# Optimization experiments

Measured on AMD Instinct MI355X. Metric: run time of the kernel, lower is better.

## Reference

```python
import jax, jax.numpy as jnp
import numpy as np

N_NODES = 50000
N_EDGES = 800000
IN_FEATS = 128
H_FEATS = 128
NUM_CLASSES = 64


def _linear_params(key, fan_in, fan_out):
    kw, kb = jax.random.split(key)
    bound = 1.0 / np.sqrt(fan_in)
    W = jax.random.uniform(kw, (fan_out, fan_in), minval=-bound, maxval=bound, dtype=jnp.float32)
    b = jax.random.uniform(kb, (fan_out,), minval=-bound, maxval=bound, dtype=jnp.float32)
    return W, b


def setup_inputs() -> dict:
    key = jax.random.key(0)
    k_feat, k_src, k_dst, k1, k2, k3 = jax.random.split(key, 6)
    in_feat = jax.random.normal(k_feat, (N_NODES, IN_FEATS), dtype=jnp.float32)
    src = jax.random.randint(k_src, (N_EDGES,), 0, N_NODES, dtype=jnp.int32)
    dst = jax.random.randint(k_dst, (N_EDGES,), 0, N_NODES, dtype=jnp.int32)
    W1, b1 = _linear_params(k1, IN_FEATS, H_FEATS)
    W2, b2 = _linear_params(k2, H_FEATS, H_FEATS)
    W3, b3 = _linear_params(k3, H_FEATS, NUM_CLASSES)
    return {"in_feat": in_feat, "W1": W1, "b1": b1, "W2": W2, "b2": b2,
            "W3": W3, "b3": b3, "src": src, "dst": dst}


def reference(in_feat, W1, b1, W2, b2, W3, b3, src, dst):
    N = in_feat.shape[0]

    def gin_layer(x, W, b):
        # DGL GINConv with eps=0: (x + sum of in-neighbor messages) -> Linear
        agg = jax.ops.segment_sum(x[src], dst, num_segments=N)  # [N, d]
        return jax.nn.relu((x + agg) @ W.T + b)

    h = gin_layer(in_feat, W1, b1)
    h = gin_layer(h, W2, b2)
    h = gin_layer(h, W3, b3)
    return h
```

## Files before the change

kernel.cpp:

```cpp
#include <hip/hip_runtime.h>

typedef _Float16 half8 __attribute__((ext_vector_type(8)));
typedef float floatx4 __attribute__((ext_vector_type(4)));
typedef unsigned int uintx4 __attribute__((ext_vector_type(4)));

union AB { uint4 u; half8 h; };
union H2 { unsigned int u; _Float16 h[2]; };
union US16 { uintx4 u[2]; unsigned short s[16]; };

#define CAPLOG 6
#define CAP 64

__global__ __launch_bounds__(256) void histA_k(const int* __restrict__ dst,
                                               int* __restrict__ histG, int E, int nbins) {
    __shared__ int h[256];
    int t = threadIdx.x;
    h[t] = 0;
    __syncthreads();
    int per = (E + 255) / 256;
    int beg = blockIdx.x * per;
    int end = min(E, beg + per);
    for (int e = beg + t; e < end; e += 256)
        atomicAdd(&h[dst[e] >> 8], 1);
    __syncthreads();
    for (int i = t; i < nbins; i += 256)
        histG[i * 256 + blockIdx.x] = h[i];
}

__global__ __launch_bounds__(1024) void scan1_k(const int* __restrict__ x,
                                                int* __restrict__ inc,
                                                int* __restrict__ partial, int n) {
    __shared__ int sd[1024];
    int t = threadIdx.x;
    int v = blockIdx.x * 1024 + t;
    sd[t] = (v < n) ? x[v] : 0;
    __syncthreads();
    for (int off = 1; off < 1024; off <<= 1) {
        int val = (t >= off) ? sd[t - off] : 0;
        __syncthreads();
        sd[t] += val;
        __syncthreads();
    }
    if (v < n) inc[v] = sd[t];
    if (t == 1023) partial[blockIdx.x] = sd[1023];
}

__global__ void scan2_k(int* __restrict__ partial, int nb) {
    int lane = threadIdx.x;
    int v = (lane < nb) ? partial[lane] : 0;
    for (int off = 1; off < 64; off <<= 1) {
        int n = __shfl_up(v, off, 64);
        if (lane >= off) v += n;
    }
    int ex = __shfl_up(v, 1, 64);
    if (lane == 0) ex = 0;
    if (lane < nb) partial[lane] = ex;
}

__global__ void scan3_excl_k(const int* __restrict__ inc, const int* __restrict__ partial,
                             const int* __restrict__ orig, int* __restrict__ excl, int n) {
    int v = blockIdx.x * blockDim.x + threadIdx.x;
    if (v < n) excl[v] = inc[v] + partial[v >> 10] - orig[v];
}

__global__ __launch_bounds__(256) void scatterA_k(const int* __restrict__ src,
                                                  const int* __restrict__ dst,
                                                  const int* __restrict__ excl,
                                                  unsigned int* __restrict__ binned,
                                                  int E, int nbins) {
    __shared__ int cur[256];
    int t = threadIdx.x;
    for (int i = t; i < nbins; i += 256) cur[i] = excl[i * 256 + blockIdx.x];
    __syncthreads();
    int per = (E + 255) / 256;
    int beg = blockIdx.x * per;
    int end = min(E, beg + per);
    for (int e = beg + t; e < end; e += 256) {
        int d = dst[e];
        int s = src[e];
        int pos = atomicAdd(&cur[d >> 8], 1);
        binned[pos] = ((unsigned int)(d & 255) << 16) | (unsigned int)s;
    }
}

__global__ __launch_bounds__(256) void binB_k(const unsigned int* __restrict__ binned,
                                              const int* __restrict__ excl,
                                              unsigned short* __restrict__ col,
                                              int* __restrict__ cnt,
                                              int N, int E, int nbins) {
    __shared__ unsigned short lcol[256 * CAP];
    __shared__ int lcnt[256];
    int t = threadIdx.x;
    int b = blockIdx.x;
    unsigned int* lcol32 = (unsigned int*)lcol;
    for (int i = t; i < 256 * CAP / 2; i += 256) lcol32[i] = 0xFFFFFFFFu;
    lcnt[t] = 0;
    __syncthreads();
    int beg = excl[b * 256];
    int end = (b == nbins - 1) ? E : excl[(b + 1) * 256];
    for (int e = beg + t; e < end; e += 256) {
        unsigned int u = binned[e];
        int dl = u >> 16;
        int pos = atomicAdd(&lcnt[dl], 1);
        if (pos < CAP) lcol[(dl << CAPLOG) + pos] = (unsigned short)(u & 0xFFFFu);
    }
    __syncthreads();
    int base = b << 8;
    int nodes = min(256, N - base);
    uint4* colg = (uint4*)(col + ((size_t)base << CAPLOG));
    const uint4* coll = (const uint4*)lcol;
    for (int i = t; i < nodes * 8; i += 256) colg[i] = coll[i];
    for (int i = t; i < nodes; i += 256) cnt[base + i] = lcnt[i];
}

__global__ void init_k(const float* __restrict__ F, const float* __restrict__ W1,
                       const float* __restrict__ W2, const float* __restrict__ W3,
                       _Float16* __restrict__ hX, _Float16* __restrict__ W1h,
                       _Float16* __restrict__ W2h, _Float16* __restrict__ W3h,
                       _Float16* __restrict__ hB,
                       int n4f, int n4w1, int n4w2, int n4w3, int zoff4) {
    int i = blockIdx.x * blockDim.x + threadIdx.x;
    const float* X;
    _Float16* O;
    int j;
    if (i < n4f) { X = F; O = hX; j = i; }
    else if (i < n4f + n4w1) { X = W1; O = W1h; j = i - n4f; }
    else if (i < n4f + n4w1 + n4w2) { X = W2; O = W2h; j = i - n4f - n4w1; }
    else if (i < n4f + n4w1 + n4w2 + n4w3) { X = W3; O = W3h; j = i - n4f - n4w1 - n4w2; }
    else {
        int z = i - (n4f + n4w1 + n4w2 + n4w3);
        if (z < 16) ((uint4*)hX)[zoff4 + z] = make_uint4(0, 0, 0, 0);
        else if (z < 32) ((uint4*)hB)[zoff4 + z - 16] = make_uint4(0, 0, 0, 0);
        return;
    }
    float4 v = reinterpret_cast<const float4*>(X)[j];
    union { uint2 u; _Float16 h[4]; } o;
    o.h[0] = (_Float16)v.x; o.h[1] = (_Float16)v.y;
    o.h[2] = (_Float16)v.z; o.h[3] = (_Float16)v.w;
    reinterpret_cast<uint2*>(O)[j] = o.u;
}

__global__ __launch_bounds__(256) void aggregate_k(const _Float16* __restrict__ X,
                                                   const int* __restrict__ cnt,
                                                   const unsigned short* __restrict__ col,
                                                   _Float16* __restrict__ Y,
                                                   int nnodes) {
    int b = blockIdx.x;
    int q = (b & 7) >> 1;
    int ng = ((b >> 3) << 1) | (b & 1);
    int lane = threadIdx.x & 63;
    int fl = lane & 15;
    int node = ng * 16 + (threadIdx.x >> 6) * 4 + (lane >> 4);
    if (node >= nnodes) return;
    const unsigned int* X32 = (const unsigned int*)X;
    int qoff = q << 4;

    int deg = cnt[node];
    if (deg > CAP) deg = CAP;
    int degp = (deg + 15) & ~15;
    const unsigned short* c = col + ((size_t)node << CAPLOG);

    float a[8], bb[8];
#pragma unroll
    for (int j = 0; j < 8; j++) { a[j] = 0.f; bb[j] = 0.f; }

    for (int e = 0; e < degp; e += 16) {
        US16 ix;
        ix.u[0] = *reinterpret_cast<const uintx4*>(c + e);
        ix.u[1] = *reinterpret_cast<const uintx4*>(c + e + 8);
        H2 u[16];
#pragma unroll
        for (int j = 0; j < 16; j++) {
            int s = (int)ix.s[j];
            s = (s < nnodes) ? s : nnodes;
            u[j].u = X32[(size_t)s * 64 + qoff + fl];
        }
#pragma unroll
        for (int j = 0; j < 8; j++) {
            a[j] += (float)u[j].h[0] + (float)u[j + 8].h[0];
            bb[j] += (float)u[j].h[1] + (float)u[j + 8].h[1];
        }
    }

    H2 xs, r;
    xs.u = X32[(size_t)node * 64 + qoff + fl];
    float s0 = ((a[0] + a[1]) + (a[2] + a[3])) + ((a[4] + a[5]) + (a[6] + a[7]));
    float s1 = ((bb[0] + bb[1]) + (bb[2] + bb[3])) + ((bb[4] + bb[5]) + (bb[6] + bb[7]));
    r.h[0] = (_Float16)((float)xs.h[0] + s0);
    r.h[1] = (_Float16)((float)xs.h[1] + s1);
    __builtin_nontemporal_store(r.u, reinterpret_cast<unsigned int*>(Y) + (size_t)node * 64 + qoff + fl);
}

template <int NOUT, bool OUT_F32>
__global__ __launch_bounds__(256) void gemm_mfma_k(const _Float16* __restrict__ Y,
                                                   const _Float16* __restrict__ Wh,
                                                   const float* __restrict__ bias,
                                                   void* __restrict__ out, int nnodes) {
    constexpr int NT = NOUT / 16;
    constexpr int WSTR = 136;
    __shared__ _Float16 Wl[NOUT * WSTR];
    __shared__ float Bl[NOUT];

    const int t = threadIdx.x;
    for (int p = t; p < NOUT * 16; p += 256) {
        int f = p >> 4;
        int kq = (p & 15) * 8;
        uint4 u = *reinterpret_cast<const uint4*>(Wh + f * 128 + kq);
        *reinterpret_cast<uint4*>(&Wl[f * WSTR + kq]) = u;
    }
    if (t < NOUT) Bl[t] = bias[t];
    __syncthreads();

    const int wave = t >> 6;
    const int lane = t & 63;
    const int quad = lane >> 4;
    const int fcol = lane & 15;
    const int m_base = (blockIdx.x * 4 + wave) * 16;
    const int row = m_base + fcol;
    const bool rowok = row < nnodes;

    floatx4 acc[NT];
#pragma unroll
    for (int ft = 0; ft < NT; ft++) acc[ft] = (floatx4){0.f, 0.f, 0.f, 0.f};

    const uint4* Yrow = reinterpret_cast<const uint4*>(Y + (size_t)row * 128);
#pragma unroll
    for (int step = 0; step < 4; step++) {
        AB a;
        if (rowok) a.u = Yrow[step * 4 + quad];
        else       a.u = make_uint4(0u, 0u, 0u, 0u);
#pragma unroll
        for (int ft = 0; ft < NT; ft++) {
            half8 b = *reinterpret_cast<const half8*>(
                &Wl[(ft * 16 + fcol) * WSTR + step * 32 + quad * 8]);
            acc[ft] = __builtin_amdgcn_mfma_f32_16x16x32_f16(a.h, b, acc[ft], 0, 0, 0);
        }
    }

#pragma unroll
    for (int ft = 0; ft < NT; ft++) {
        int f = ft * 16 + fcol;
        float bv = Bl[f];
#pragma unroll
        for (int r = 0; r < 4; r++) {
            int node = m_base + quad * 4 + r;
            if (node < nnodes) {
                float v = fmaxf(acc[ft][r] + bv, 0.f);
                if (OUT_F32)
                    reinterpret_cast<float*>(out)[(size_t)node * NOUT + f] = v;
                else
                    reinterpret_cast<_Float16*>(out)[(size_t)node * NOUT + f] = (_Float16)v;
            }
        }
    }
}

extern "C" void kernel_launch(void* const* d_in, const int* in_sizes, int n_in,
                              void* d_out, int out_size, void* d_ws, size_t ws_size,
                              hipStream_t stream) {
    const float* in_feat = (const float*)d_in[0];
    const float* W1 = (const float*)d_in[1];
    const float* b1 = (const float*)d_in[2];
    const float* W2 = (const float*)d_in[3];
    const float* b2 = (const float*)d_in[4];
    const float* W3 = (const float*)d_in[5];
    const float* b3 = (const float*)d_in[6];
    const int* src = (const int*)d_in[7];
    const int* dst = (const int*)d_in[8];
    float* out = (float*)d_out;

    const int N = in_sizes[0] / 128;
    const int E = in_sizes[7];
    const int szW1 = in_sizes[1];
    const int szW2 = in_sizes[3];
    const int szW3 = in_sizes[5];
    const int nbins = (N + 255) >> 8;
    const int nhist = nbins * 256;

    char* p = (char*)d_ws;
    int* cnt = (int*)p;               p += (size_t)N * 4;
    unsigned short* col = (unsigned short*)p; p += (size_t)N * CAP * 2;
    int* histG = (int*)p;             p += (size_t)nhist * 4;
    int* incS = (int*)p;              p += (size_t)nhist * 4;
    int* excl = (int*)p;              p += (size_t)nhist * 4;
    int* partial = (int*)p;           p += 256;
    unsigned int* binned = (unsigned int*)p; p += (size_t)E * 4;
    _Float16* hX = (_Float16*)p;      p += (size_t)(N + 1) * 128 * 2;
    _Float16* hB = (_Float16*)p;      p += (size_t)(N + 1) * 128 * 2;
    _Float16* W1h = (_Float16*)p;     p += (size_t)szW1 * 2;
    _Float16* W2h = (_Float16*)p;     p += (size_t)szW2 * 2;
    _Float16* W3h = (_Float16*)p;     p += (size_t)szW3 * 2;

    const int nblk_scan = (nhist + 1023) / 1024;

    histA_k<<<256, 256, 0, stream>>>(dst, histG, E, nbins);
    scan1_k<<<nblk_scan, 1024, 0, stream>>>(histG, incS, partial, nhist);
    scan2_k<<<1, 64, 0, stream>>>(partial, nblk_scan);
    scan3_excl_k<<<(nhist + 255) / 256, 256, 0, stream>>>(incS, partial, histG, excl, nhist);
    scatterA_k<<<256, 256, 0, stream>>>(src, dst, excl, binned, E, nbins);
    binB_k<<<nbins, 256, 0, stream>>>(binned, excl, col, cnt, N, E, nbins);

    {
        int n4f = N * 128 / 4;
        int total = n4f + szW1 / 4 + szW2 / 4 + szW3 / 4 + 32;
        init_k<<<(total + 255) / 256, 256, 0, stream>>>(in_feat, W1, W2, W3,
                                                        hX, W1h, W2h, W3h, hB,
                                                        n4f, szW1 / 4, szW2 / 4, szW3 / 4,
                                                        N * 16);
    }

    const int ngrp = (N + 15) / 16;
    const int nblk_agg = 8 * ((ngrp + 1) / 2);
    const int nblk_gemm = (N + 63) / 64;
    aggregate_k<<<nblk_agg, 256, 0, stream>>>(hX, cnt, col, hB, N);
    gemm_mfma_k<128, false><<<nblk_gemm, 256, 0, stream>>>(hB, W1h, b1, hX, N);
    aggregate_k<<<nblk_agg, 256, 0, stream>>>(hX, cnt, col, hB, N);
    gemm_mfma_k<128, false><<<nblk_gemm, 256, 0, stream>>>(hB, W2h, b2, hX, N);
    aggregate_k<<<nblk_agg, 256, 0, stream>>>(hX, cnt, col, hB, N);
    gemm_mfma_k<64, true><<<nblk_gemm, 256, 0, stream>>>(hB, W3h, b3, out, N);
}
```

Measured before the change: 263.9 us.

## Reorder last GIN layer to GEMM-then-aggregate and fuse preprocessing kernels

For the final layer the code now applies the linear map first, (x+agg)W = xW + agg(xW), so the last aggregation gathers 64-wide fp16 rows instead of 128-wide. Bias and ReLU move into a new final aggregation kernel that writes fp32 output. The histogram and fp16 conversion kernels are merged into one launch, and the scan2/scan3 steps are folded into the scatter and binning kernels, removing several small launches. The aggregate kernel's mapping changes from quarter-row to half-row chunks per thread group with a different XCD-aware block swizzle. The reordering changes fp16 rounding order, since the GEMM output is rounded before summation.

```diff
diff --git a/kernel.cpp b/kernel.cpp
--- a/kernel.cpp
+++ b/kernel.cpp
@@ -11,115 +11,30 @@
 #define CAPLOG 6
 #define CAP 64
 
-__global__ __launch_bounds__(256) void histA_k(const int* __restrict__ dst,
-                                               int* __restrict__ histG, int E, int nbins) {
-    __shared__ int h[256];
+__global__ __launch_bounds__(256) void histA_init_k(
+    const int* __restrict__ dst, int* __restrict__ histG, int E, int nbins,
+    const float* __restrict__ F, const float* __restrict__ W1,
+    const float* __restrict__ W2, const float* __restrict__ W3,
+    _Float16* __restrict__ hX, _Float16* __restrict__ W1h,
+    _Float16* __restrict__ W2h, _Float16* __restrict__ W3h,
+    _Float16* __restrict__ hZ,
+    int n4f, int n4w1, int n4w2, int n4w3, int zoffX4, int zoffZ4) {
     int t = threadIdx.x;
-    h[t] = 0;
-    __syncthreads();
-    int per = (E + 255) / 256;
-    int beg = blockIdx.x * per;
-    int end = min(E, beg + per);
-    for (int e = beg + t; e < end; e += 256)
-        atomicAdd(&h[dst[e] >> 8], 1);
-    __syncthreads();
-    for (int i = t; i < nbins; i += 256)
-        histG[i * 256 + blockIdx.x] = h[i];
-}
-
-__global__ __launch_bounds__(1024) void scan1_k(const int* __restrict__ x,
-                                                int* __restrict__ inc,
-                                                int* __restrict__ partial, int n) {
-    __shared__ int sd[1024];
-    int t = threadIdx.x;
-    int v = blockIdx.x * 1024 + t;
-    sd[t] = (v < n) ? x[v] : 0;
-    __syncthreads();
-    for (int off = 1; off < 1024; off <<= 1) {
-        int val = (t >= off) ? sd[t - off] : 0;
+    if (blockIdx.x < 256) {
+        __shared__ int h[256];
+        h[t] = 0;
         __syncthreads();
-        sd[t] += val;
+        int per = (E + 255) / 256;
+        int beg = blockIdx.x * per;
+        int end = min(E, beg + per);
+        for (int e = beg + t; e < end; e += 256)
+            atomicAdd(&h[dst[e] >> 8], 1);
         __syncthreads();
-    }
-    if (v < n) inc[v] = sd[t];
-    if (t == 1023) partial[blockIdx.x] = sd[1023];
-}
-
-__global__ void scan2_k(int* __restrict__ partial, int nb) {
-    int lane = threadIdx.x;
-    int v = (lane < nb) ? partial[lane] : 0;
-    for (int off = 1; off < 64; off <<= 1) {
-        int n = __shfl_up(v, off, 64);
-        if (lane >= off) v += n;
-    }
-    int ex = __shfl_up(v, 1, 64);
-    if (lane == 0) ex = 0;
-    if (lane < nb) partial[lane] = ex;
-}
-
-__global__ void scan3_excl_k(const int* __restrict__ inc, const int* __restrict__ partial,
-                             const int* __restrict__ orig, int* __restrict__ excl, int n) {
-    int v = blockIdx.x * blockDim.x + threadIdx.x;
-    if (v < n) excl[v] = inc[v] + partial[v >> 10] - orig[v];
-}
-
-__global__ __launch_bounds__(256) void scatterA_k(const int* __restrict__ src,
-                                                  const int* __restrict__ dst,
-                                                  const int* __restrict__ excl,
-                                                  unsigned int* __restrict__ binned,
-                                                  int E, int nbins) {
-    __shared__ int cur[256];
-    int t = threadIdx.x;
-    for (int i = t; i < nbins; i += 256) cur[i] = excl[i * 256 + blockIdx.x];
-    __syncthreads();
-    int per = (E + 255) / 256;
-    int beg = blockIdx.x * per;
-    int end = min(E, beg + per);
-    for (int e = beg + t; e < end; e += 256) {
-        int d = dst[e];
-        int s = src[e];
-        int pos = atomicAdd(&cur[d >> 8], 1);
-        binned[pos] = ((unsigned int)(d & 255) << 16) | (unsigned int)s;
-    }
-}
-
-__global__ __launch_bounds__(256) void binB_k(const unsigned int* __restrict__ binned,
-                                              const int* __restrict__ excl,
-                                              unsigned short* __restrict__ col,
-                                              int* __restrict__ cnt,
-                                              int N, int E, int nbins) {
-    __shared__ unsigned short lcol[256 * CAP];
-    __shared__ int lcnt[256];
-    int t = threadIdx.x;
-    int b = blockIdx.x;
-    unsigned int* lcol32 = (unsigned int*)lcol;
-    for (int i = t; i < 256 * CAP / 2; i += 256) lcol32[i] = 0xFFFFFFFFu;
-    lcnt[t] = 0;
-    __syncthreads();
-    int beg = excl[b * 256];
-    int end = (b == nbins - 1) ? E : excl[(b + 1) * 256];
-    for (int e = beg + t; e < end; e += 256) {
-        unsigned int u = binned[e];
-        int dl = u >> 16;
-        int pos = atomicAdd(&lcnt[dl], 1);
-        if (pos < CAP) lcol[(dl << CAPLOG) + pos] = (unsigned short)(u & 0xFFFFu);
-    }
-    __syncthreads();
-    int base = b << 8;
-    int nodes = min(256, N - base);
-    uint4* colg = (uint4*)(col + ((size_t)base << CAPLOG));
-    const uint4* coll = (const uint4*)lcol;
-    for (int i = t; i < nodes * 8; i += 256) colg[i] = coll[i];
-    for (int i = t; i < nodes; i += 256) cnt[base + i] = lcnt[i];
-}
-
-__global__ void init_k(const float* __restrict__ F, const float* __restrict__ W1,
-                       const float* __restrict__ W2, const float* __restrict__ W3,
-                       _Float16* __restrict__ hX, _Float16* __restrict__ W1h,
-                       _Float16* __restrict__ W2h, _Float16* __restrict__ W3h,
-                       _Float16* __restrict__ hB,
-                       int n4f, int n4w1, int n4w2, int n4w3, int zoff4) {
-    int i = blockIdx.x * blockDim.x + threadIdx.x;
+        for (int i = t; i < nbins; i += 256)
+            histG[i * 256 + blockIdx.x] = h[i];
+        return;
+    }
+    int i = (blockIdx.x - 256) * 256 + t;
     const float* X;
     _Float16* O;
     int j;
@@ -129,8 +44,8 @@
     else if (i < n4f + n4w1 + n4w2 + n4w3) { X = W3; O = W3h; j = i - n4f - n4w1 - n4w2; }
     else {
         int z = i - (n4f + n4w1 + n4w2 + n4w3);
-        if (z < 16) ((uint4*)hX)[zoff4 + z] = make_uint4(0, 0, 0, 0);
-        else if (z < 32) ((uint4*)hB)[zoff4 + z - 16] = make_uint4(0, 0, 0, 0);
+        if (z < 16) ((uint4*)hX)[zoffX4 + z] = make_uint4(0, 0, 0, 0);
+        else if (z < 24) ((uint4*)hZ)[zoffZ4 + (z - 16)] = make_uint4(0, 0, 0, 0);
         return;
     }
     float4 v = reinterpret_cast<const float4*>(X)[j];
@@ -138,6 +53,115 @@
     o.h[0] = (_Float16)v.x; o.h[1] = (_Float16)v.y;
     o.h[2] = (_Float16)v.z; o.h[3] = (_Float16)v.w;
     reinterpret_cast<uint2*>(O)[j] = o.u;
+}
+
+__global__ __launch_bounds__(1024) void scan1_k(const int* __restrict__ x,
+                                                int* __restrict__ inc,
+                                                int* __restrict__ partial, int n) {
+    __shared__ int sd[1024];
+    int t = threadIdx.x;
+    int v = blockIdx.x * 1024 + t;
+    sd[t] = (v < n) ? x[v] : 0;
+    __syncthreads();
+    for (int off = 1; off < 1024; off <<= 1) {
+        int val = (t >= off) ? sd[t - off] : 0;
+        __syncthreads();
+        sd[t] += val;
+        __syncthreads();
+    }
+    if (v < n) inc[v] = sd[t];
+    if (t == 1023) partial[blockIdx.x] = sd[1023];
+}
+
+__global__ __launch_bounds__(256) void scatterB_k(const int* __restrict__ src,
+                                                  const int* __restrict__ dst,
+                                                  const int* __restrict__ inc,
+                                                  const int* __restrict__ histG,
+                                                  const int* __restrict__ partial, int nparts,
+                                                  unsigned int* __restrict__ binned,
+                                                  int E, int nbins) {
+    __shared__ int cur[256];
+    __shared__ int pp[64];
+    int t = threadIdx.x, blk = blockIdx.x;
+    if (t < 64) {
+        int v = (t < nparts) ? partial[t] : 0;
+        for (int off = 1; off < 64; off <<= 1) {
+            int n = __shfl_up(v, off, 64);
+            if (t >= off) v += n;
+        }
+        int ex = __shfl_up(v, 1, 64);
+        if (t == 0) ex = 0;
+        pp[t] = ex;
+    }
+    __syncthreads();
+    for (int i = t; i < nbins; i += 256) {
+        int idx = i * 256 + blk;
+        cur[i] = inc[idx] + pp[idx >> 10] - histG[idx];
+    }
+    __syncthreads();
+    int per = (E + 255) / 256;
+    int beg = blk * per;
+    int end = min(E, beg + per);
+    for (int e = beg + t; e < end; e += 256) {
+        int d = dst[e];
+        int s = src[e];
+        int pos = atomicAdd(&cur[d >> 8], 1);
+        binned[pos] = ((unsigned int)(d & 255) << 16) | (unsigned int)s;
+    }
+}
+
+__global__ __launch_bounds__(256) void binB_k(const unsigned int* __restrict__ binned,
+                                              const int* __restrict__ inc,
+                                              const int* __restrict__ histG,
+                                              const int* __restrict__ partial, int nparts,
+                                              unsigned short* __restrict__ col,
+                                              int* __restrict__ cnt,
+                                              int N, int E, int nbins) {
+    __shared__ unsigned short lcol[256 * CAP];
+    __shared__ int lcnt[256];
+    __shared__ int pp[64];
+    __shared__ int bounds[2];
+    int t = threadIdx.x;
+    int b = blockIdx.x;
+    if (t < 64) {
+        int v = (t < nparts) ? partial[t] : 0;
+        for (int off = 1; off < 64; off <<= 1) {
+            int n = __shfl_up(v, off, 64);
+            if (t >= off) v += n;
+        }
+        int ex = __shfl_up(v, 1, 64);
+        if (t == 0) ex = 0;
+        pp[t] = ex;
+    }
+    unsigned int* lcol32 = (unsigned int*)lcol;
+    for (int i = t; i < 256 * CAP / 2; i += 256) lcol32[i] = 0xFFFFFFFFu;
+    lcnt[t] = 0;
+    __syncthreads();
+    if (t == 0) {
+        int i0 = b * 256;
+        bounds[0] = inc[i0] + pp[i0 >> 10] - histG[i0];
+    } else if (t == 1) {
+        if (b == nbins - 1) bounds[1] = E;
+        else {
+            int i1 = (b + 1) * 256;
+            bounds[1] = inc[i1] + pp[i1 >> 10] - histG[i1];
+        }
+    }
+    __syncthreads();
+    int beg = bounds[0], end = bounds[1];
+    for (int e = beg + t; e < end; e += 256) {
+        unsigned int u = binned[e];
+        int dl = u >> 16;
+        int pos = atomicAdd(&lcnt[dl], 1);
+        if (pos < CAP) lcol[(dl << CAPLOG) + pos] = (unsigned short)(u & 0xFFFFu);
+    }
+    __syncthreads();
+    int base = b << 8;
+    int nodes = min(256, N - base);
+    uint4* colg = (uint4*)(col + ((size_t)base << CAPLOG));
+    const uint4* coll = (const uint4*)lcol;
+    for (int i = t; i < nodes * 8; i += 256) colg[i] = coll[i];
+    for (int i = t; i < nodes; i += 256) cnt[base + i] = lcnt[i];
 }
 
 __global__ __launch_bounds__(256) void aggregate_k(const _Float16* __restrict__ X,
@@ -146,14 +170,15 @@
                                                    _Float16* __restrict__ Y,
                                                    int nnodes) {
     int b = blockIdx.x;
-    int q = (b & 7) >> 1;
-    int ng = ((b >> 3) << 1) | (b & 1);
+    int xcd = b & 7;
+    int h = xcd >> 2;
+    int ng = (b >> 3) * 4 + (xcd & 3);
     int lane = threadIdx.x & 63;
-    int fl = lane & 15;
-    int node = ng * 16 + (threadIdx.x >> 6) * 4 + (lane >> 4);
+    int fl = lane & 31;
+    int node = ng * 8 + (threadIdx.x >> 6) * 2 + (lane >> 5);
     if (node >= nnodes) return;
     const unsigned int* X32 = (const unsigned int*)X;
-    int qoff = q << 4;
+    int hoff = h << 5;
 
     int deg = cnt[node];
     if (deg > CAP) deg = CAP;
@@ -173,7 +198,7 @@
         for (int j = 0; j < 16; j++) {
             int s = (int)ix.s[j];
             s = (s < nnodes) ? s : nnodes;
-            u[j].u = X32[(size_t)s * 64 + qoff + fl];
+            u[j].u = X32[(size_t)s * 64 + hoff + fl];
         }
 #pragma unroll
         for (int j = 0; j < 8; j++) {
@@ -183,19 +208,68 @@
     }
 
     H2 xs, r;
-    xs.u = X32[(size_t)node * 64 + qoff + fl];
+    xs.u = X32[(size_t)node * 64 + hoff + fl];
     float s0 = ((a[0] + a[1]) + (a[2] + a[3])) + ((a[4] + a[5]) + (a[6] + a[7]));
     float s1 = ((bb[0] + bb[1]) + (bb[2] + bb[3])) + ((bb[4] + bb[5]) + (bb[6] + bb[7]));
     r.h[0] = (_Float16)((float)xs.h[0] + s0);
     r.h[1] = (_Float16)((float)xs.h[1] + s1);
-    __builtin_nontemporal_store(r.u, reinterpret_cast<unsigned int*>(Y) + (size_t)node * 64 + qoff + fl);
-}
-
-template <int NOUT, bool OUT_F32>
+    __builtin_nontemporal_store(r.u, reinterpret_cast<unsigned int*>(Y) + (size_t)node * 64 + hoff + fl);
+}
+
+__global__ __launch_bounds__(256) void agg_final_k(const _Float16* __restrict__ Z,
+                                                   const int* __restrict__ cnt,
+                                                   const unsigned short* __restrict__ col,
+                                                   const float* __restrict__ bias,
+                                                   float* __restrict__ out, int nnodes) {
+    int lane = threadIdx.x & 63;
+    int fl = lane & 31;
+    int node = blockIdx.x * 8 + (threadIdx.x >> 6) * 2 + (lane >> 5);
+    if (node >= nnodes) return;
+    const unsigned int* Z32 = (const unsigned int*)Z;
+
+    int deg = cnt[node];
+    if (deg > CAP) deg = CAP;
+    int degp = (deg + 15) & ~15;
+    const unsigned short* c = col + ((size_t)node << CAPLOG);
+
+    float a[8], bb[8];
+#pragma unroll
+    for (int j = 0; j < 8; j++) { a[j] = 0.f; bb[j] = 0.f; }
+
+    for (int e = 0; e < degp; e += 16) {
+        US16 ix;
+        ix.u[0] = *reinterpret_cast<const uintx4*>(c + e);
+        ix.u[1] = *reinterpret_cast<const uintx4*>(c + e + 8);
+        H2 u[16];
+#pragma unroll
+        for (int j = 0; j < 16; j++) {
+            int s = (int)ix.s[j];
+            s = (s < nnodes) ? s : nnodes;
+            u[j].u = Z32[(size_t)s * 32 + fl];
+        }
+#pragma unroll
+        for (int j = 0; j < 8; j++) {
+            a[j] += (float)u[j].h[0] + (float)u[j + 8].h[0];
+            bb[j] += (float)u[j].h[1] + (float)u[j + 8].h[1];
+        }
+    }
+
+    H2 xs;
+    xs.u = Z32[(size_t)node * 32 + fl];
+    float2 bv = reinterpret_cast<const float2*>(bias)[fl];
+    float s0 = ((a[0] + a[1]) + (a[2] + a[3])) + ((a[4] + a[5]) + (a[6] + a[7]));
+    float s1 = ((bb[0] + bb[1]) + (bb[2] + bb[3])) + ((bb[4] + bb[5]) + (bb[6] + bb[7]));
+    float2 r;
+    r.x = fmaxf((float)xs.h[0] + s0 + bv.x, 0.f);
+    r.y = fmaxf((float)xs.h[1] + s1 + bv.y, 0.f);
+    reinterpret_cast<float2*>(out)[(size_t)node * 32 + fl] = r;
+}
+
+template <int NOUT, bool RAW>
 __global__ __launch_bounds__(256) void gemm_mfma_k(const _Float16* __restrict__ Y,
                                                    const _Float16* __restrict__ Wh,
                                                    const float* __restrict__ bias,
-                                                   void* __restrict__ out, int nnodes) {
+                                                   _Float16* __restrict__ out, int nnodes) {
     constexpr int NT = NOUT / 16;
     constexpr int WSTR = 136;
     __shared__ _Float16 Wl[NOUT * WSTR];
@@ -208,7 +282,7 @@
         uint4 u = *reinterpret_cast<const uint4*>(Wh + f * 128 + kq);
         *reinterpret_cast<uint4*>(&Wl[f * WSTR + kq]) = u;
     }
-    if (t < NOUT) Bl[t] = bias[t];
+    if (!RAW && t < NOUT) Bl[t] = bias[t];
     __syncthreads();
 
     const int wave = t >> 6;
@@ -240,16 +314,14 @@
 #pragma unroll
     for (int ft = 0; ft < NT; ft++) {
         int f = ft * 16 + fcol;
-        float bv = Bl[f];
+        float bv = RAW ? 0.f : Bl[f];
 #pragma unroll
         for (int r = 0; r < 4; r++) {
             int node = m_base + quad * 4 + r;
             if (node < nnodes) {
-                float v = fmaxf(acc[ft][r] + bv, 0.f);
-                if (OUT_F32)
-                    reinterpret_cast<float*>(out)[(size_t)node * NOUT + f] = v;
-                else
-                    reinterpret_cast<_Float16*>(out)[(size_t)node * NOUT + f] = (_Float16)v;
+                float v = acc[ft][r] + bv;
+                if (!RAW) v = fmaxf(v, 0.f);
+                out[(size_t)node * NOUT + f] = (_Float16)v;
             }
         }
     }
@@ -282,40 +354,40 @@
     unsigned short* col = (unsigned short*)p; p += (size_t)N * CAP * 2;
     int* histG = (int*)p;             p += (size_t)nhist * 4;
     int* incS = (int*)p;              p += (size_t)nhist * 4;
-    int* excl = (int*)p;              p += (size_t)nhist * 4;
     int* partial = (int*)p;           p += 256;
     unsigned int* binned = (unsigned int*)p; p += (size_t)E * 4;
     _Float16* hX = (_Float16*)p;      p += (size_t)(N + 1) * 128 * 2;
-    _Float16* hB = (_Float16*)p;      p += (size_t)(N + 1) * 128 * 2;
+    _Float16* hB = (_Float16*)p;      p += (size_t)N * 128 * 2;
+    _Float16* hZ = (_Float16*)p;      p += (size_t)(N + 1) * 64 * 2;
     _Float16* W1h = (_Float16*)p;     p += (size_t)szW1 * 2;
     _Float16* W2h = (_Float16*)p;     p += (size_t)szW2 * 2;
     _Float16* W3h = (_Float16*)p;     p += (size_t)szW3 * 2;
 
     const int nblk_scan = (nhist + 1023) / 1024;
 
-    histA_k<<<256, 256, 0, stream>>>(dst, histG, E, nbins);
-    scan1_k<<<nblk_scan, 1024, 0, stream>>>(histG, incS, partial, nhist);
-    scan2_k<<<1, 64, 0, stream>>>(partial, nblk_scan);
-    scan3_excl_k<<<(nhist + 255) / 256, 256, 0, stream>>>(incS, partial, histG, excl, nhist);
-    scatterA_k<<<256, 256, 0, stream>>>(src, dst, excl, binned, E, nbins);
-    binB_k<<<nbins, 256, 0, stream>>>(binned, excl, col, cnt, N, E, nbins);
-
     {
         int n4f = N * 128 / 4;
         int total = n4f + szW1 / 4 + szW2 / 4 + szW3 / 4 + 32;
-        init_k<<<(total + 255) / 256, 256, 0, stream>>>(in_feat, W1, W2, W3,
-                                                        hX, W1h, W2h, W3h, hB,
-                                                        n4f, szW1 / 4, szW2 / 4, szW3 / 4,
-                                                        N * 16);
-    }
-
-    const int ngrp = (N + 15) / 16;
-    const int nblk_agg = 8 * ((ngrp + 1) / 2);
+        int iblk = (total + 255) / 256;
+        histA_init_k<<<256 + iblk, 256, 0, stream>>>(dst, histG, E, nbins,
+                                                     in_feat, W1, W2, W3,
+                                                     hX, W1h, W2h, W3h, hZ,
+                                                     n4f, szW1 / 4, szW2 / 4, szW3 / 4,
+                                                     N * 16, N * 8);
+    }
+    scan1_k<<<nblk_scan, 1024, 0, stream>>>(histG, incS, partial, nhist);
+    scatterB_k<<<256, 256, 0, stream>>>(src, dst, incS, histG, partial, nblk_scan,
+                                        binned, E, nbins);
+    binB_k<<<nbins, 256, 0, stream>>>(binned, incS, histG, partial, nblk_scan,
+                                      col, cnt, N, E, nbins);
+
+    const int ngrp8 = (N + 7) / 8;
+    const int nblk_agg = ((ngrp8 + 3) / 4) * 8;
     const int nblk_gemm = (N + 63) / 64;
     aggregate_k<<<nblk_agg, 256, 0, stream>>>(hX, cnt, col, hB, N);
     gemm_mfma_k<128, false><<<nblk_gemm, 256, 0, stream>>>(hB, W1h, b1, hX, N);
     aggregate_k<<<nblk_agg, 256, 0, stream>>>(hX, cnt, col, hB, N);
     gemm_mfma_k<128, false><<<nblk_gemm, 256, 0, stream>>>(hB, W2h, b2, hX, N);
-    aggregate_k<<<nblk_agg, 256, 0, stream>>>(hX, cnt, col, hB, N);
-    gemm_mfma_k<64, true><<<nblk_gemm, 256, 0, stream>>>(hB, W3h, b3, out, N);
-}
+    gemm_mfma_k<64, true><<<nblk_gemm, 256, 0, stream>>>(hX, W3h, nullptr, hZ, N);
+    agg_final_k<<<(N + 7) / 8, 256, 0, stream>>>(hZ, cnt, col, b3, out, N);
+}
```

Measured after the change: 264.3 us. Within noise of the previous version (+0.1%).
